# Kernel tuning notes

Hardware: AMD Instinct MI355X
Metric: run time of the kernel (lower is better)

## Reference

```python
import jax, jax.numpy as jnp
import numpy as np
import math

B, S, E, H = 4, 2048, 1024, 16
D = E // H
INFINITY = 1000000.0

def setup_inputs() -> dict:
    key = jax.random.key(0)
    ks = jax.random.split(key, 10)
    std = 1.0 / math.sqrt(E)
    inp = {
        "x": jax.random.normal(ks[0], (B, S, E), dtype=jnp.float32),
        "mask": jax.random.randint(ks[1], (B, S), 0, 2).astype(jnp.bool_),
        "WQ_w": jax.random.uniform(ks[2], (E, E), jnp.float32, -std, std),
        "WQ_b": jax.random.uniform(ks[3], (E,), jnp.float32, -std, std),
        "WK_w": jax.random.uniform(ks[4], (E, E), jnp.float32, -std, std),
        "WK_b": jax.random.uniform(ks[5], (E,), jnp.float32, -std, std),
        "WV_w": jax.random.uniform(ks[6], (E, E), jnp.float32, -std, std),
        "WV_b": jax.random.uniform(ks[7], (E,), jnp.float32, -std, std),
        "WO_w": jax.random.uniform(ks[8], (E, E), jnp.float32, -std, std),
        "WO_b": jax.random.uniform(ks[9], (E,), jnp.float32, -std, std),
    }
    return inp

def reference(x, mask, WQ_w, WQ_b, WK_w, WK_b, WV_w, WV_b, WO_w, WO_b):
    # Linear layers: y = x @ W.T + b (torch convention)
    q = (x @ WQ_w.T + WQ_b).reshape(B, S, H, D).transpose(0, 2, 1, 3)  # (B,H,S,D)
    k = (x @ WK_w.T + WK_b).reshape(B, S, H, D).transpose(0, 2, 1, 3)
    v = (x @ WV_w.T + WV_b).reshape(B, S, H, D).transpose(0, 2, 1, 3)
    score = jnp.einsum("bhqd,bhkd->bhqk", q, k) / math.sqrt(D)  # (B,H,S,S)
    # additive key mask: -infinity where mask is False
    inv_mask = (~mask).astype(jnp.float32)[:, None, None, :]  # (B,1,1,S)
    score = score - inv_mask * INFINITY
    attn = jax.nn.softmax(score, axis=-1)
    o = jnp.einsum("bhqk,bhkd->bhqd", attn, v)  # (B,H,S,D)
    o = o.transpose(0, 2, 1, 3).reshape(B, S, E)
    o = o @ WO_w.T + WO_b
    o = jnp.abs(o * mask.astype(jnp.float32)[:, :, None])
    return o
```

## Files before the change

kernel.cpp:

```cpp
#include <hip/hip_runtime.h>
#include <math.h>

#define B_ 4
#define S_ 2048
#define E_ 1024
#define H_ 16
#define D_ 64
#define MTOT (B_*S_)

typedef _Float16 half8v __attribute__((ext_vector_type(8)));
typedef _Float16 half4v __attribute__((ext_vector_type(4)));
typedef float f32x4 __attribute__((ext_vector_type(4)));
typedef float f32x16 __attribute__((ext_vector_type(16)));
typedef unsigned uint4v __attribute__((ext_vector_type(4)));

typedef __attribute__((address_space(1))) const void gconst_void;
typedef __attribute__((address_space(3))) void lds_void;

#define MFMA16(a,b,c) __builtin_amdgcn_mfma_f32_16x16x32_f16((a),(b),(c),0,0,0)
#define MFMA32(a,b,c) __builtin_amdgcn_mfma_f32_32x32x16_f16((a),(b),(c),0,0,0)

#define QSCALE 0.18033688011112042f

static __device__ __forceinline__ unsigned cvt_pk_u32(float a, float b) {
  return __builtin_bit_cast(unsigned, __builtin_amdgcn_cvt_pkrtz(a, b));
}

#if __has_builtin(__builtin_amdgcn_permlane32_swap)
static __device__ __forceinline__ void pl32_swap(unsigned a, unsigned b,
                                                 unsigned& rlo, unsigned& rhi) {
  auto r = __builtin_amdgcn_permlane32_swap(a, b, false, false);
  rlo = r[0]; rhi = r[1];
}
#else
static __device__ __forceinline__ void pl32_swap(unsigned a, unsigned b,
                                                 unsigned& rlo, unsigned& rhi) {
  const int hi = (threadIdx.x & 63) >> 5;
  unsigned t = __shfl_xor(hi ? a : b, 32);
  rlo = hi ? t : a;
  rhi = hi ? b : t;
}
#endif

static __device__ __forceinline__ float partner32(float v, int hi) {
  unsigned u = __builtin_bit_cast(unsigned, v);
  unsigned lo_, hi_;
  pl32_swap(u, u, lo_, hi_);
  return __builtin_bit_cast(float, hi ? lo_ : hi_);
}

__global__ __launch_bounds__(256) void cvt_w4(const float* __restrict__ w0, const float* __restrict__ w1,
                                              const float* __restrict__ w2, const float* __restrict__ w3,
                                              _Float16* __restrict__ o0, _Float16* __restrict__ o1,
                                              _Float16* __restrict__ o2, _Float16* __restrict__ o3) {
  const int z = blockIdx.y;
  const float* in = (z == 0) ? w0 : (z == 1) ? w1 : (z == 2) ? w2 : w3;
  _Float16* out = (z == 0) ? o0 : (z == 1) ? o1 : (z == 2) ? o2 : o3;
  int i = (blockIdx.x * 256 + threadIdx.x) * 4;
  float4 v = *(const float4*)(in + i);
  half4v o;
  o[0] = (_Float16)v.x; o[1] = (_Float16)v.y; o[2] = (_Float16)v.z; o[3] = (_Float16)v.w;
  *(half4v*)(out + i) = o;
}

__global__ __launch_bounds__(256) void zero_out(float* __restrict__ out) {
  const size_t i = ((size_t)blockIdx.x * 256 + threadIdx.x) * 4;
  float4 z = make_float4(0.f, 0.f, 0.f, 0.f);
  *(float4*)(out + i) = z;
}

__global__ __launch_bounds__(256) void mask_prep(const unsigned char* __restrict__ mraw,
                                                 _Float16* __restrict__ maskc,
                                                 float* __restrict__ qmask,
                                                 int* __restrict__ ks,
                                                 int* __restrict__ nkpa) {
  __shared__ int flags[2];
  __shared__ int psum[256];
  const int b = blockIdx.x, tid = threadIdx.x;
  if (tid < 2) flags[tid] = 1;
  __syncthreads();
  const unsigned int* w = (const unsigned int*)mraw;
  for (int i = tid; i < 2048; i += 256) {
    unsigned int v = w[i];
    if (!(v == 0u || v == 1u)) flags[0] = 0;
    if (!(v == 0u || v == 0x3f800000u)) flags[1] = 0;
  }
  __syncthreads();
  const int is_i32 = flags[0], is_f32 = flags[1];
  int m[8]; int cnt = 0;
  for (int i = 0; i < 8; ++i) {
    const int idx = b * 2048 + tid * 8 + i;
    int mv;
    if (is_i32)      mv = ((const int*)mraw)[idx];
    else if (is_f32) mv = (((const unsigned int*)mraw)[idx] != 0u);
    else             mv = (mraw[idx] != 0);
    m[i] = mv; cnt += mv;
    qmask[idx] = mv ? 1.0f : 0.0f;
  }
  psum[tid] = cnt;
  __syncthreads();
  for (int off = 1; off < 256; off <<= 1) {
    int u = (tid >= off) ? psum[tid - off] : 0;
    __syncthreads();
    psum[tid] += u;
    __syncthreads();
  }
  const int total = psum[255];
  int base = psum[tid] - cnt;
  for (int i = 0; i < 8; ++i)
    if (m[i]) ks[b * 2048 + (base++)] = tid * 8 + i;
  for (int j = tid; j < 2048; j += 256)
    maskc[b * 2048 + j] = (j < total) ? (_Float16)0.0f : (_Float16)(-60000.0f);
  __syncthreads();
  const int lastv = (total > 0) ? ks[b * 2048 + total - 1] : 0;
  for (int j = total + tid; j < 2048; j += 256)
    ks[b * 2048 + j] = lastv;
  if (tid == 0) nkpa[b] = (total + 127) & ~127;
}

__global__ __launch_bounds__(256) void cvt_xc(const float* __restrict__ x,
                                              const int* __restrict__ ks,
                                              const int* __restrict__ nkpa,
                                              _Float16* __restrict__ xc) {
  const int b = blockIdx.y, j = blockIdx.x;
  if (j >= nkpa[b]) return;
  const int s = ks[b * 2048 + j];
  const float* src = x + (size_t)(b * 2048 + s) * E_;
  _Float16* dst = xc + (size_t)(b * 2048 + j) * E_;
  const int i = threadIdx.x * 4;
  float4 v = *(const float4*)(src + i);
  half4v o;
  o[0] = (_Float16)v.x; o[1] = (_Float16)v.y; o[2] = (_Float16)v.z; o[3] = (_Float16)v.w;
  *(half4v*)(dst + i) = o;
}

__device__ __forceinline__ void stage128x32(const _Float16* __restrict__ g, int ld,
                                            _Float16* lds, int wid, int lane) {
#pragma unroll
  for (int j = 0; j < 2; ++j) {
    const int c = j * 256 + wid * 64 + lane;
    const _Float16* src = g + (size_t)(c >> 2) * ld + (c & 3) * 8;
    _Float16* dst = lds + (size_t)(j * 256 + wid * 64) * 8;
    __builtin_amdgcn_global_load_lds((gconst_void*)src, (lds_void*)dst, 16, 0, 0);
  }
}

__global__ __launch_bounds__(256) void qkv_gemm(
    const _Float16* __restrict__ xc, const int* __restrict__ nkpa,
    const _Float16* __restrict__ wq, const _Float16* __restrict__ wk, const _Float16* __restrict__ wv,
    const float* __restrict__ bq, const float* __restrict__ bkp, const float* __restrict__ bvp,
    _Float16* __restrict__ Qc, _Float16* __restrict__ Kc, _Float16* __restrict__ Vc) {
  const int id = blockIdx.x;
  const int tt = id / 96;
  const int rem = id % 96;
  const int bb = rem / 24;
  const int r2 = rem % 24;
  const int by = r2 / 3, z = r2 % 3;
  if (tt * 128 >= nkpa[bb]) return;
  __shared__ _Float16 As[128 * 32];
  __shared__ _Float16 Bs[128 * 32];
  const int tid = threadIdx.x, lane = tid & 63, wid = tid >> 6;
  const int g = lane >> 4, r16 = lane & 15;
  const int bm = (bb * 16 + tt) * 128, bn = by * 128;
  const _Float16* w = (z == 0) ? wq : (z == 1) ? wk : wv;
  const float* bias = (z == 0) ? bq : (z == 1) ? bkp : bvp;
  const int wr = wid >> 1, wc = wid & 1;
  f32x4 acc[4][4] = {};
  for (int k0 = 0; k0 < E_; k0 += 32) {
    stage128x32(xc + (size_t)bm * E_ + k0, E_, As, wid, lane);
    stage128x32(w + (size_t)bn * E_ + k0, E_, Bs, wid, lane);
    __syncthreads();
    half8v a[4], bf[4];
#pragma unroll
    for (int i = 0; i < 4; ++i) a[i] = *(const half8v*)&As[(wr * 64 + i * 16 + r16) * 32 + g * 8];
#pragma unroll
    for (int i = 0; i < 4; ++i) bf[i] = *(const half8v*)&Bs[(wc * 64 + i * 16 + r16) * 32 + g * 8];
#pragma unroll
    for (int i = 0; i < 4; ++i)
#pragma unroll
      for (int j = 0; j < 4; ++j) acc[i][j] = MFMA16(a[i], bf[j], acc[i][j]);
    __syncthreads();
  }
#pragma unroll
  for (int i = 0; i < 4; ++i) {
#pragma unroll
    for (int j = 0; j < 4; ++j) {
      const int gn = bn + wc * 64 + j * 16 + r16;
      const float bb2 = bias[gn];
      const int h = gn >> 6, d = gn & 63;
      const int gm0 = bm + wr * 64 + i * 16 + g * 4;
      const int b_ = gm0 >> 11, s0 = gm0 & (S_ - 1);
      const size_t bhbase = (size_t)(b_ * H_ + h) * S_ * D_;
      if (z == 2) {
        half4v v4;
#pragma unroll
        for (int ii = 0; ii < 4; ++ii) v4[ii] = (_Float16)(acc[i][j][ii] + bb2);
        *(half4v*)&Vc[bhbase + (size_t)(s0 >> 4) * (D_ * 16) + d * 16 + (s0 & 15)] = v4;
      } else if (z == 1) {
#pragma unroll
        for (int ii = 0; ii < 4; ++ii) {
          const int s = s0 + ii;
          Kc[bhbase + (size_t)(s >> 5) * 2048 + (d >> 4) * 512 + (s & 31) * 16 + (d & 15)] =
              (_Float16)(acc[i][j][ii] + bb2);
        }
      } else {
#pragma unroll
        for (int ii = 0; ii < 4; ++ii)
          Qc[bhbase + (size_t)(s0 + ii) * D_ + d] = (_Float16)((acc[i][j][ii] + bb2) * QSCALE);
      }
    }
  }
}

__global__ __launch_bounds__(512) void attn_kernel(
    const _Float16* __restrict__ Qc, const _Float16* __restrict__ Kc, const _Float16* __restrict__ Vc,
    const _Float16* __restrict__ maskc, const int* __restrict__ nkpa,
    _Float16* __restrict__ Oc) {
  __shared__ float mlds[4][64][36];
  _Float16* smask = (_Float16*)&mlds[0][0][0];
  const int tid = threadIdx.x, lane = tid & 63, wid = tid >> 6;
  const int c = lane & 31, hi = lane >> 5;
  const int qg = wid & 3, kh = wid >> 2;
  const int id = blockIdx.x;
  const int slot = id & 7, hbh = (id >> 3) & 7, t = id >> 6;
  const int hb = hbh * 8 + slot;
  const int b = hb >> 4, h = hb & 15;
  const int nkp = nkpa[b];
  if (t * 128 >= nkp) return;
  const size_t bh = (size_t)(b * H_ + h);
  const _Float16* Qb = Qc + bh * S_ * D_;
  const _Float16* Kb = Kc + bh * S_ * D_;
  const _Float16* Vb = Vc + bh * S_ * D_;

  *((half4v*)smask + tid) = *((const half4v*)(maskc + (size_t)b * S_) + tid);

  const int jq = t * 128 + qg * 32 + c;

  half8v qb[4];
#pragma unroll
  for (int kc = 0; kc < 4; ++kc)
    qb[kc] = *(const half8v*)&Qb[(size_t)jq * D_ + 16 * kc + 8 * hi];

  half8v bone = {};
  if (hi == 0) bone[0] = (_Float16)1.0f;
  const f32x16 fzero = {};

  f32x16 oacc[2] = {};
  float mrun = -1e30f, lrun = 0.f;
  const int laneoff = c * 16 + 8 * hi;
  const int nkh = nkp >> 1;
  const int kb0 = kh * nkh;

  __syncthreads();

  half8v kaf[4];
  {
    const _Float16* ktb = Kb + (size_t)(kb0 >> 5) * 2048 + laneoff;
#pragma unroll
    for (int kc = 0; kc < 4; ++kc) kaf[kc] = *(const half8v*)&ktb[kc * 512];
  }
  _Float16 mv = smask[kb0 + c];

  for (int kb = kb0; kb < kb0 + nkh; kb += 32) {
    half8v amask = {};
    if (hi == 0) amask[0] = mv;
    __builtin_amdgcn_s_setprio(1);
    f32x16 sc = MFMA32(amask, bone, fzero);
    sc = MFMA32(kaf[0], qb[0], sc);
    sc = MFMA32(kaf[1], qb[1], sc);
    sc = MFMA32(kaf[2], qb[2], sc);
    sc = MFMA32(kaf[3], qb[3], sc);
    __builtin_amdgcn_s_setprio(0);
    const int kbn = (kb + 32 < kb0 + nkh) ? kb + 32 : kb0;
    {
      const _Float16* ktb = Kb + (size_t)(kbn >> 5) * 2048 + laneoff;
#pragma unroll
      for (int kc = 0; kc < 4; ++kc) kaf[kc] = *(const half8v*)&ktb[kc * 512];
    }
    mv = smask[kbn + c];
    const _Float16* v_base = Vb + (size_t)(kb >> 4) * (D_ * 16) + laneoff;
    half8v va00 = *(const half8v*)&v_base[0];
    half8v va01 = *(const half8v*)&v_base[512];
    half8v va10 = *(const half8v*)&v_base[1024];
    half8v va11 = *(const half8v*)&v_base[1024 + 512];
    float t0 = fmaxf(sc[0], sc[4]), t1 = fmaxf(sc[1], sc[5]);
    float t2 = fmaxf(sc[2], sc[6]), t3 = fmaxf(sc[3], sc[7]);
    t0 = fmaxf(fmaxf(sc[8], sc[12]), t0);
    t1 = fmaxf(fmaxf(sc[9], sc[13]), t1);
    t2 = fmaxf(fmaxf(sc[10], sc[14]), t2);
    t3 = fmaxf(fmaxf(sc[11], sc[15]), t3);
    float pmax = fmaxf(fmaxf(t0, t1), fmaxf(t2, t3));
    pmax = fmaxf(pmax, partner32(pmax, hi));
    if (__any(pmax > mrun + 11.0f)) {
      float mnew = fmaxf(mrun, pmax);
      float corr = __builtin_amdgcn_exp2f(mrun - mnew);
      mrun = mnew;
      lrun *= corr;
#pragma unroll
      for (int dt = 0; dt < 2; ++dt)
#pragma unroll
        for (int r = 0; r < 16; ++r) oacc[dt][r] *= corr;
    }
    float ps0 = 0.f, ps1 = 0.f;
#pragma unroll
    for (int sl = 0; sl < 2; ++sl) {
      const int bs = 8 * sl;
      float p0 = __builtin_amdgcn_exp2f(sc[bs + 0] - mrun);
      float p1 = __builtin_amdgcn_exp2f(sc[bs + 1] - mrun);
      float p2 = __builtin_amdgcn_exp2f(sc[bs + 2] - mrun);
      float p3 = __builtin_amdgcn_exp2f(sc[bs + 3] - mrun);
      float p4 = __builtin_amdgcn_exp2f(sc[bs + 4] - mrun);
      float p5 = __builtin_amdgcn_exp2f(sc[bs + 5] - mrun);
      float p6 = __builtin_amdgcn_exp2f(sc[bs + 6] - mrun);
      float p7 = __builtin_amdgcn_exp2f(sc[bs + 7] - mrun);
      ps0 += (p0 + p1) + (p2 + p3);
      ps1 += (p4 + p5) + (p6 + p7);
      unsigned uA = cvt_pk_u32(p0, p1);
      unsigned uB = cvt_pk_u32(p2, p3);
      unsigned uC = cvt_pk_u32(p4, p5);
      unsigned uD = cvt_pk_u32(p6, p7);
      unsigned w0, w1, w2, w3;
      pl32_swap(uA, uC, w0, w2);
      pl32_swap(uB, uD, w1, w3);
      uint4v u4 = {w0, w1, w2, w3};
      half8v pb = __builtin_bit_cast(half8v, u4);
      __builtin_amdgcn_s_setprio(1);
      oacc[0] = MFMA32(sl ? va10 : va00, pb, oacc[0]);
      oacc[1] = MFMA32(sl ? va11 : va01, pb, oacc[1]);
      __builtin_amdgcn_s_setprio(0);
    }
    lrun += ps0 + ps1;
  }
  lrun += partner32(lrun, hi);
  __syncthreads();
  if (kh == 1) {
    float* p = &mlds[qg][lane][0];
#pragma unroll
    for (int dt = 0; dt < 2; ++dt)
#pragma unroll
      for (int rr = 0; rr < 4; ++rr) {
        float4 v4 = make_float4(oacc[dt][4 * rr], oacc[dt][4 * rr + 1],
                                oacc[dt][4 * rr + 2], oacc[dt][4 * rr + 3]);
        *(float4*)&p[dt * 16 + rr * 4] = v4;
      }
    p[32] = mrun;
    p[33] = lrun;
  }
  __syncthreads();
  if (kh == 0) {
    const float* p = &mlds[qg][lane][0];
    const float mB = p[32], lB = p[33];
    const float mS = fmaxf(mrun, mB);
    const float cA = __builtin_amdgcn_exp2f(mrun - mS);
    const float cB = __builtin_amdgcn_exp2f(mB - mS);
    const float inv = 1.0f / (lrun * cA + lB * cB);
    const float fA = cA * inv, fB = cB * inv;
    _Float16* orow = Oc + ((size_t)(b * S_ + jq)) * E_ + h * D_;
#pragma unroll
    for (int dt = 0; dt < 2; ++dt)
#pragma unroll
      for (int rr = 0; rr < 4; ++rr) {
        float4 vB = *(const float4*)&p[dt * 16 + rr * 4];
        half4v o4;
        o4[0] = (_Float16)(oacc[dt][4 * rr + 0] * fA + vB.x * fB);
        o4[1] = (_Float16)(oacc[dt][4 * rr + 1] * fA + vB.y * fB);
        o4[2] = (_Float16)(oacc[dt][4 * rr + 2] * fA + vB.z * fB);
        o4[3] = (_Float16)(oacc[dt][4 * rr + 3] * fA + vB.w * fB);
        *(half4v*)&orow[32 * dt + 8 * rr + 4 * hi] = o4;
      }
  }
}

__global__ __launch_bounds__(256) void oproj_gemm(
    const _Float16* __restrict__ Oc, const _Float16* __restrict__ wo, const float* __restrict__ bo,
    const int* __restrict__ ks, const int* __restrict__ nkpa, float* __restrict__ out) {
  const int id = blockIdx.x;
  const int tt = id / 32;
  const int rem = id % 32;
  const int bb = rem / 8, by = rem % 8;
  if (tt * 128 >= nkpa[bb]) return;
  __shared__ _Float16 As[128 * 32];
  __shared__ _Float16 Bs[128 * 32];
  const int tid = threadIdx.x, lane = tid & 63, wid = tid >> 6;
  const int g = lane >> 4, r16 = lane & 15;
  const int bm = (bb * 16 + tt) * 128, bn = by * 128;
  const int wr = wid >> 1, wc = wid & 1;
  f32x4 acc[4][4] = {};
  for (int k0 = 0; k0 < E_; k0 += 32) {
    stage128x32(Oc + (size_t)bm * E_ + k0, E_, As, wid, lane);
    stage128x32(wo + (size_t)bn * E_ + k0, E_, Bs, wid, lane);
    __syncthreads();
    half8v a[4], bf[4];
#pragma unroll
    for (int i = 0; i < 4; ++i) a[i] = *(const half8v*)&As[(wr * 64 + i * 16 + r16) * 32 + g * 8];
#pragma unroll
    for (int i = 0; i < 4; ++i) bf[i] = *(const half8v*)&Bs[(wc * 64 + i * 16 + r16) * 32 + g * 8];
#pragma unroll
    for (int i = 0; i < 4; ++i)
#pragma unroll
      for (int j = 0; j < 4; ++j) acc[i][j] = MFMA16(a[i], bf[j], acc[i][j]);
    __syncthreads();
  }
#pragma unroll
  for (int i = 0; i < 4; ++i) {
#pragma unroll
    for (int j = 0; j < 4; ++j) {
      const int gn = bn + wc * 64 + j * 16 + r16;
      const float bb2 = bo[gn];
      const int gm0 = bm + wr * 64 + i * 16 + g * 4;
#pragma unroll
      for (int ii = 0; ii < 4; ++ii) {
        const int gm = gm0 + ii;
        const int b_ = gm >> 11, j_ = gm & (S_ - 1);
        const int sorig = ks[b_ * 2048 + j_];
        const float y = acc[i][j][ii] + bb2;
        out[((size_t)(b_ * S_ + sorig)) * E_ + gn] = fabsf(y);
      }
    }
  }
}

extern "C" void kernel_launch(void* const* d_in, const int* in_sizes, int n_in,
                              void* d_out, int out_size, void* d_ws, size_t ws_size,
                              hipStream_t stream) {
  const float* x = (const float*)d_in[0];
  const unsigned char* mask = (const unsigned char*)d_in[1];
  const float* WQ_w = (const float*)d_in[2];
  const float* WQ_b = (const float*)d_in[3];
  const float* WK_w = (const float*)d_in[4];
  const float* WK_b = (const float*)d_in[5];
  const float* WV_w = (const float*)d_in[6];
  const float* WV_b = (const float*)d_in[7];
  const float* WO_w = (const float*)d_in[8];
  const float* WO_b = (const float*)d_in[9];

  char* ws = (char*)d_ws;
  size_t off = 0;
  _Float16* xc  = (_Float16*)(ws + off); off += (size_t)MTOT * E_ * 2;
  _Float16* wqh = (_Float16*)(ws + off); off += (size_t)E_ * E_ * 2;
  _Float16* wkh = (_Float16*)(ws + off); off += (size_t)E_ * E_ * 2;
  _Float16* wvh = (_Float16*)(ws + off); off += (size_t)E_ * E_ * 2;
  _Float16* woh = (_Float16*)(ws + off); off += (size_t)E_ * E_ * 2;
  _Float16* Qc  = (_Float16*)(ws + off); off += (size_t)MTOT * E_ * 2;
  _Float16* Kc  = (_Float16*)(ws + off); off += (size_t)MTOT * E_ * 2;
  _Float16* Vc  = (_Float16*)(ws + off); off += (size_t)MTOT * E_ * 2;
  _Float16* Oc  = (_Float16*)(ws + off); off += (size_t)MTOT * E_ * 2;
  _Float16* maskcf = (_Float16*)(ws + off); off += (size_t)B_ * S_ * 2;
  float* qmaskf = (float*)(ws + off); off += (size_t)B_ * S_ * 4;
  int* ksl      = (int*)(ws + off); off += (size_t)B_ * S_ * 4;
  int* nkpa     = (int*)(ws + off); off += 64;
  if (ws_size < off) return;

  const int NW = E_ * E_;
  mask_prep<<<dim3(B_), dim3(256), 0, stream>>>(mask, maskcf, qmaskf, ksl, nkpa);
  cvt_w4<<<dim3(NW / 4 / 256, 4), dim3(256), 0, stream>>>(WQ_w, WK_w, WV_w, WO_w,
                                                          wqh, wkh, wvh, woh);
  cvt_xc<<<dim3(S_, B_), dim3(256), 0, stream>>>(x, ksl, nkpa, xc);
  zero_out<<<dim3(MTOT * E_ / 4 / 256), dim3(256), 0, stream>>>((float*)d_out);
  qkv_gemm<<<dim3(16 * B_ * 8 * 3), dim3(256), 0, stream>>>(
      xc, nkpa, wqh, wkh, wvh, WQ_b, WK_b, WV_b, Qc, Kc, Vc);
  attn_kernel<<<dim3((S_ / 128) * H_ * B_), dim3(512), 0, stream>>>(
      Qc, Kc, Vc, maskcf, nkpa, Oc);
  oproj_gemm<<<dim3(16 * B_ * 8), dim3(256), 0, stream>>>(Oc, woh, WO_b, ksl, nkpa, (float*)d_out);
}
```

Measured before the change: 150.6 us.

## Use K=64 XOR-swizzled LDS tiles in GEMMs and shrink oproj M tile

Both projection GEMMs now stage 64-wide K slices instead of 32. The LDS layout is XOR-swizzled by row so the half8 fragment reads avoid bank conflicts, and each loop iteration now feeds two MFMA sub-steps. This halves the number of barrier pairs per tile. The output projection also drops to 64-row M tiles, doubling its grid so more blocks run on the CUs, at the cost of reloading the weight tile more often. The qkv grid constant of 1536 equals the old expression, so its block count is unchanged.

Result: faster. 136.2 us (-9.6%).

```diff
diff --git a/kernel.cpp b/kernel.cpp
--- a/kernel.cpp
+++ b/kernel.cpp
@@ -134,12 +134,15 @@
   *(half4v*)(dst + i) = o;
 }
 
-__device__ __forceinline__ void stage128x32(const _Float16* __restrict__ g, int ld,
-                                            _Float16* lds, int wid, int lane) {
-#pragma unroll
-  for (int j = 0; j < 2; ++j) {
+template <int ROWS>
+__device__ __forceinline__ void stageX64s(const _Float16* __restrict__ g, int ld,
+                                          _Float16* lds, int wid, int lane) {
+#pragma unroll
+  for (int j = 0; j < ROWS / 32; ++j) {
     const int c = j * 256 + wid * 64 + lane;
-    const _Float16* src = g + (size_t)(c >> 2) * ld + (c & 3) * 8;
+    const int row = c >> 3, dslot = c & 7;
+    const int sslot = dslot ^ (row & 7);
+    const _Float16* src = g + (size_t)row * ld + sslot * 8;
     _Float16* dst = lds + (size_t)(j * 256 + wid * 64) * 8;
     __builtin_amdgcn_global_load_lds((gconst_void*)src, (lds_void*)dst, 16, 0, 0);
   }
@@ -157,28 +160,33 @@
   const int r2 = rem % 24;
   const int by = r2 / 3, z = r2 % 3;
   if (tt * 128 >= nkpa[bb]) return;
-  __shared__ _Float16 As[128 * 32];
-  __shared__ _Float16 Bs[128 * 32];
+  __shared__ _Float16 As[128 * 64];
+  __shared__ _Float16 Bs[128 * 64];
   const int tid = threadIdx.x, lane = tid & 63, wid = tid >> 6;
   const int g = lane >> 4, r16 = lane & 15;
   const int bm = (bb * 16 + tt) * 128, bn = by * 128;
   const _Float16* w = (z == 0) ? wq : (z == 1) ? wk : wv;
   const float* bias = (z == 0) ? bq : (z == 1) ? bkp : bvp;
   const int wr = wid >> 1, wc = wid & 1;
+  const int sw = r16 & 7;
   f32x4 acc[4][4] = {};
-  for (int k0 = 0; k0 < E_; k0 += 32) {
-    stage128x32(xc + (size_t)bm * E_ + k0, E_, As, wid, lane);
-    stage128x32(w + (size_t)bn * E_ + k0, E_, Bs, wid, lane);
-    __syncthreads();
-    half8v a[4], bf[4];
-#pragma unroll
-    for (int i = 0; i < 4; ++i) a[i] = *(const half8v*)&As[(wr * 64 + i * 16 + r16) * 32 + g * 8];
-#pragma unroll
-    for (int i = 0; i < 4; ++i) bf[i] = *(const half8v*)&Bs[(wc * 64 + i * 16 + r16) * 32 + g * 8];
-#pragma unroll
-    for (int i = 0; i < 4; ++i)
-#pragma unroll
-      for (int j = 0; j < 4; ++j) acc[i][j] = MFMA16(a[i], bf[j], acc[i][j]);
+  for (int k0 = 0; k0 < E_; k0 += 64) {
+    stageX64s<128>(xc + (size_t)bm * E_ + k0, E_, As, wid, lane);
+    stageX64s<128>(w + (size_t)bn * E_ + k0, E_, Bs, wid, lane);
+    __syncthreads();
+#pragma unroll
+    for (int kk = 0; kk < 2; ++kk) {
+      const int so = ((kk * 4 + g) ^ sw) * 8;
+      half8v a[4], bf[4];
+#pragma unroll
+      for (int i = 0; i < 4; ++i) a[i] = *(const half8v*)&As[(wr * 64 + i * 16 + r16) * 64 + so];
+#pragma unroll
+      for (int j = 0; j < 4; ++j) bf[j] = *(const half8v*)&Bs[(wc * 64 + j * 16 + r16) * 64 + so];
+#pragma unroll
+      for (int i = 0; i < 4; ++i)
+#pragma unroll
+        for (int j = 0; j < 4; ++j) acc[i][j] = MFMA16(a[i], bf[j], acc[i][j]);
+    }
     __syncthreads();
   }
 #pragma unroll
@@ -375,39 +383,44 @@
     const _Float16* __restrict__ Oc, const _Float16* __restrict__ wo, const float* __restrict__ bo,
     const int* __restrict__ ks, const int* __restrict__ nkpa, float* __restrict__ out) {
   const int id = blockIdx.x;
-  const int tt = id / 32;
+  const int jt = id / 32;
   const int rem = id % 32;
   const int bb = rem / 8, by = rem % 8;
-  if (tt * 128 >= nkpa[bb]) return;
-  __shared__ _Float16 As[128 * 32];
-  __shared__ _Float16 Bs[128 * 32];
+  if (jt * 64 >= nkpa[bb]) return;
+  __shared__ _Float16 As[64 * 64];
+  __shared__ _Float16 Bs[128 * 64];
   const int tid = threadIdx.x, lane = tid & 63, wid = tid >> 6;
   const int g = lane >> 4, r16 = lane & 15;
-  const int bm = (bb * 16 + tt) * 128, bn = by * 128;
+  const int bm = bb * 2048 + jt * 64, bn = by * 128;
   const int wr = wid >> 1, wc = wid & 1;
-  f32x4 acc[4][4] = {};
-  for (int k0 = 0; k0 < E_; k0 += 32) {
-    stage128x32(Oc + (size_t)bm * E_ + k0, E_, As, wid, lane);
-    stage128x32(wo + (size_t)bn * E_ + k0, E_, Bs, wid, lane);
-    __syncthreads();
-    half8v a[4], bf[4];
-#pragma unroll
-    for (int i = 0; i < 4; ++i) a[i] = *(const half8v*)&As[(wr * 64 + i * 16 + r16) * 32 + g * 8];
-#pragma unroll
-    for (int i = 0; i < 4; ++i) bf[i] = *(const half8v*)&Bs[(wc * 64 + i * 16 + r16) * 32 + g * 8];
-#pragma unroll
-    for (int i = 0; i < 4; ++i)
-#pragma unroll
-      for (int j = 0; j < 4; ++j) acc[i][j] = MFMA16(a[i], bf[j], acc[i][j]);
-    __syncthreads();
-  }
-#pragma unroll
-  for (int i = 0; i < 4; ++i) {
+  const int sw = r16 & 7;
+  f32x4 acc[2][4] = {};
+  for (int k0 = 0; k0 < E_; k0 += 64) {
+    stageX64s<64>(Oc + (size_t)bm * E_ + k0, E_, As, wid, lane);
+    stageX64s<128>(wo + (size_t)bn * E_ + k0, E_, Bs, wid, lane);
+    __syncthreads();
+#pragma unroll
+    for (int kk = 0; kk < 2; ++kk) {
+      const int so = ((kk * 4 + g) ^ sw) * 8;
+      half8v a[2], bf[4];
+#pragma unroll
+      for (int i = 0; i < 2; ++i) a[i] = *(const half8v*)&As[(wr * 32 + i * 16 + r16) * 64 + so];
+#pragma unroll
+      for (int j = 0; j < 4; ++j) bf[j] = *(const half8v*)&Bs[(wc * 64 + j * 16 + r16) * 64 + so];
+#pragma unroll
+      for (int i = 0; i < 2; ++i)
+#pragma unroll
+        for (int j = 0; j < 4; ++j) acc[i][j] = MFMA16(a[i], bf[j], acc[i][j]);
+    }
+    __syncthreads();
+  }
+#pragma unroll
+  for (int i = 0; i < 2; ++i) {
 #pragma unroll
     for (int j = 0; j < 4; ++j) {
       const int gn = bn + wc * 64 + j * 16 + r16;
       const float bb2 = bo[gn];
-      const int gm0 = bm + wr * 64 + i * 16 + g * 4;
+      const int gm0 = bm + wr * 32 + i * 16 + g * 4;
 #pragma unroll
       for (int ii = 0; ii < 4; ++ii) {
         const int gm = gm0 + ii;
@@ -457,9 +470,9 @@
                                                           wqh, wkh, wvh, woh);
   cvt_xc<<<dim3(S_, B_), dim3(256), 0, stream>>>(x, ksl, nkpa, xc);
   zero_out<<<dim3(MTOT * E_ / 4 / 256), dim3(256), 0, stream>>>((float*)d_out);
-  qkv_gemm<<<dim3(16 * B_ * 8 * 3), dim3(256), 0, stream>>>(
+  qkv_gemm<<<dim3(1536), dim3(256), 0, stream>>>(
       xc, nkpa, wqh, wkh, wvh, WQ_b, WK_b, WV_b, Qc, Kc, Vc);
   attn_kernel<<<dim3((S_ / 128) * H_ * B_), dim3(512), 0, stream>>>(
       Qc, Kc, Vc, maskcf, nkpa, Oc);
-  oproj_gemm<<<dim3(16 * B_ * 8), dim3(256), 0, stream>>>(Oc, woh, WO_b, ksl, nkpa, (float*)d_out);
-}
+  oproj_gemm<<<dim3(32 * 32), dim3(256), 0, stream>>>(Oc, woh, WO_b, ksl, nkpa, (float*)d_out);
+}
```
